# Optimization experiments

Hardware: AMD Instinct MI355X
Metric: run time of the kernel (lower is better)

The kernel has to match this reference:

```python
import jax, jax.numpy as jnp
import numpy as np

B, N = 2, 1024
D, H, DK, L = 128, 8, 16, 4
K_GCN, K_LOC, COARSE = 16, 8, 512
EPS = 1e-5
SCALE = 1.0 / float(np.sqrt(DK))


def _dist2(q, r):
    # squared euclidean distances [Nq, Nr]; same ordering as torch.cdist for topk
    return jnp.sum(q * q, -1)[:, None] - 2.0 * (q @ r.T) + jnp.sum(r * r, -1)[None, :]


def _knn_self(coords, k):
    # knn_graph(loop=False): k nearest neighbors excluding self, per batch
    def one(c):
        d2 = _dist2(c, c) + jnp.eye(c.shape[0], dtype=c.dtype) * 1e10
        return jax.lax.top_k(-d2, k)[1]  # [N, k] source-node indices
    return jax.vmap(one)(coords)


def _gcn(x, idx, w, b, k):
    # PyG GCNConv with self-loops on a knn graph: target in-degree is uniformly k+1,
    # so gcn_norm reduces to mean over {self} U knn neighbors.
    nb = jax.vmap(lambda xb, ib: xb[ib])(x, idx)  # [B,N,k,C]
    agg = (x + nb.sum(2)) / float(k + 1)
    return agg @ w + b


def _ln(x, g, b):
    m = x.mean(-1, keepdims=True)
    v = ((x - m) ** 2).mean(-1, keepdims=True)
    return (x - m) * jax.lax.rsqrt(v + EPS) * g + b


def _neigh_mean(part, pred, k):
    # local_knn + mean over the k gathered partial neighbors
    def one(pb, qb):
        idx = jax.lax.top_k(-_dist2(qb, pb), k)[1]  # [Nq,k]
        return pb[idx].mean(1)                      # [Nq,3]
    return jax.vmap(one)(part, pred)


def _refine(part, pred, sw1, sb1, sw2, sb2, dw, db, cw, cb):
    # LocalRefineStage: seed MLP -> ConvTranspose1d(k=2,s=2) on length-1 seq -> 1x1 conv -> offsets
    nm = _neigh_mean(part, pred, K_LOC)
    comb = jnp.concatenate([pred, nm], -1)                          # [B,N,6]
    seed = jax.nn.relu(comb @ sw1 + sb1) @ sw2 + sb2                # [B,N,128]
    h = jax.nn.relu(jnp.einsum('bnc,cot->bnot', seed, dw) + db[:, None])  # [B,N,128,2]
    y = jnp.einsum('bnot,po->bntp', h, cw) + cb                     # [B,N,2,3]
    child = pred[:, :, None, :] + y
    return child.reshape(pred.shape[0], -1, 3)


def _forward(partial_coords, gcn_w0, gcn_b0, gcn_w1, gcn_b1, enc_fw, enc_fb,
             t_wq, t_bq, t_wk, t_bk, t_wv, t_bv, t_alpha,
             t_f1w, t_f1b, t_f2w, t_f2b, t_ln1g, t_ln1b, t_ln2g, t_ln2b,
             dec_w1, dec_b1, dec_w2, dec_b2,
             st_sw1, st_sb1, st_sw2, st_sb2, st_dw, st_db, st_cw, st_cb):
    coords = partial_coords
    # --- GraphEncoder ---
    idx = _knn_self(coords, K_GCN)
    x = jax.nn.relu(_gcn(coords, idx, gcn_w0, gcn_b0, K_GCN))
    x = jax.nn.relu(_gcn(x, idx, gcn_w1, gcn_b1, K_GCN))
    x = x @ enc_fw + enc_fb  # tokens [B,N,128]; bridge_in is Identity (128==128)
    # --- GeomMultiTokenTransformer ---
    # block-diagonal extraction of (coords coords^T) == per-batch dot-product bias
    G = jnp.einsum('bnc,bmc->bnm', coords, coords)
    for i in range(L):
        q = (x @ t_wq[i] + t_bq[i]).reshape(B, N, H, DK)
        k = (x @ t_wk[i] + t_bk[i]).reshape(B, N, H, DK)
        v = (x @ t_wv[i] + t_bv[i]).reshape(B, N, H, DK)
        scores = jnp.einsum('bnhd,bmhd->bhnm', q, k) * SCALE + (t_alpha[i] * G)[:, None]
        a = jax.nn.softmax(scores, axis=-1)
        attn = jnp.einsum('bhnm,bmhd->bnhd', a, v).reshape(B, N, D)
        x = _ln(x + attn, t_ln1g[i], t_ln1b[i])
        ff = jax.nn.relu(x @ t_f1w[i] + t_f1b[i]) @ t_f2w[i] + t_f2b[i]
        x = _ln(x + ff, t_ln2g[i], t_ln2b[i])
    # --- Snowflake3StageDecoder ---
    gc = x.mean(1)
    pts = (jax.nn.relu(gc @ dec_w1 + dec_b1) @ dec_w2 + dec_b2).reshape(B, COARSE, 3)
    for s in range(3):
        pts = _refine(coords, pts, st_sw1[s], st_sb1[s], st_sw2[s], st_sb2[s],
                      st_dw[s], st_db[s], st_cw[s], st_cb[s])
    return pts  # [B, 4096, 3]


def setup_inputs() -> dict:
    key = jax.random.key(0)
    it = iter(jax.random.split(key, 64))
    def w(*shape):
        return jax.random.normal(next(it), shape, dtype=jnp.float32) * 0.05
    z = lambda *s: jnp.zeros(s, dtype=jnp.float32)
    o = lambda *s: jnp.ones(s, dtype=jnp.float32)
    return {
        'partial_coords': jax.random.normal(next(it), (B, N, 3), dtype=jnp.float32),
        'gcn_w0': w(3, 64), 'gcn_b0': z(64),
        'gcn_w1': w(64, 128), 'gcn_b1': z(128),
        'enc_fw': w(128, 128), 'enc_fb': z(128),
        't_wq': w(L, D, D), 't_bq': z(L, D),
        't_wk': w(L, D, D), 't_bk': z(L, D),
        't_wv': w(L, D, D), 't_bv': z(L, D),
        't_alpha': jnp.full((L,), 0.1, dtype=jnp.float32),
        't_f1w': w(L, D, 4 * D), 't_f1b': z(L, 4 * D),
        't_f2w': w(L, 4 * D, D), 't_f2b': z(L, D),
        't_ln1g': o(L, D), 't_ln1b': z(L, D),
        't_ln2g': o(L, D), 't_ln2b': z(L, D),
        'dec_w1': w(128, 128), 'dec_b1': z(128),
        'dec_w2': w(128, 3 * COARSE), 'dec_b2': z(3 * COARSE),
        'st_sw1': w(3, 6, 128), 'st_sb1': z(3, 128),
        'st_sw2': w(3, 128, 128), 'st_sb2': z(3, 128),
        'st_dw': w(3, 128, 128, 2), 'st_db': z(3, 128),
        'st_cw': w(3, 3, 128), 'st_cb': z(3, 3),
    }


def reference(partial_coords, gcn_w0, gcn_b0, gcn_w1, gcn_b1, enc_fw, enc_fb,
              t_wq, t_bq, t_wk, t_bk, t_wv, t_bv, t_alpha,
              t_f1w, t_f1b, t_f2w, t_f2b, t_ln1g, t_ln1b, t_ln2g, t_ln2b,
              dec_w1, dec_b1, dec_w2, dec_b2,
              st_sw1, st_sb1, st_sw2, st_sb2, st_dw, st_db, st_cw, st_cb):
    return _forward(partial_coords, gcn_w0, gcn_b0, gcn_w1, gcn_b1, enc_fw, enc_fb,
                    t_wq, t_bq, t_wk, t_bk, t_wv, t_bv, t_alpha,
                    t_f1w, t_f1b, t_f2w, t_f2b, t_ln1g, t_ln1b, t_ln2g, t_ln2b,
                    dec_w1, dec_b1, dec_w2, dec_b2,
                    st_sw1, st_sb1, st_sw2, st_sb2, st_dw, st_db, st_cw, st_cb)
```

## Files before the change

### kernel.cpp

```cpp
#include <hip/hip_runtime.h>


#define B_ 2
#define N_ 1024
#define D_ 128
#define H_ 8
#define DK_ 16
#define L_ 4
#define KG_ 16
#define KLOC_ 8
#define COARSE_ 512
#define AW_ 8
#define KSP_ 4
#define PREC_ 17
#define QPL_ 4

static __device__ __forceinline__ float wave_sum(float v) {
    #pragma unroll
    for (int off = 32; off > 0; off >>= 1) v += __shfl_xor(v, off);
    return v;
}
static __device__ __forceinline__ float half_sum(float v) {
    #pragma unroll
    for (int off = 16; off > 0; off >>= 1) v += __shfl_xor(v, off);
    return v;
}

template <int CIN, bool RELU, bool BIAS_HALF>
static __device__ __forceinline__ float4 gemm_body(
        const float* __restrict__ X, const float* __restrict__ W,
        const float* __restrict__ bias, int wstride, int col0) {
    __shared__ float Xs[8 * CIN];
    __shared__ float Ws[64][128];
    int tid = threadIdx.x;
    int row0 = blockIdx.x * 8;
    constexpr int NX4 = 2 * CIN;
    {
        const float4* xg = (const float4*)(X + (size_t)row0 * CIN);
        float4* xs4 = (float4*)Xs;
        #pragma unroll
        for (int i = 0; i < (NX4 + 255) / 256; ++i) {
            int t = tid + i * 256;
            if ((NX4 % 256 == 0) || t < NX4) xs4[t] = xg[t];
        }
    }
    int col4 = (tid & 31) << 2;
    int rowl = tid >> 5;
    float4 acc;
    if (BIAS_HALF) {
        acc.x = bias[(col0 + col4) >> 1];
        acc.y = bias[(col0 + col4 + 1) >> 1];
        acc.z = bias[(col0 + col4 + 2) >> 1];
        acc.w = bias[(col0 + col4 + 3) >> 1];
    } else {
        acc = *(const float4*)(bias + col0 + col4);
    }
    for (int c0 = 0; c0 < CIN; c0 += 64) {
        __syncthreads();
        #pragma unroll
        for (int i = 0; i < 8; ++i) {
            int flat = tid + i * 256;
            int wr = flat >> 5, wc = (flat & 31) << 2;
            *(float4*)&Ws[wr][wc] =
                *(const float4*)(W + (size_t)(c0 + wr) * wstride + col0 + wc);
        }
        __syncthreads();
        const float* xrow = Xs + rowl * CIN + c0;
        #pragma unroll
        for (int c = 0; c < 64; ++c) {
            float xv = xrow[c];
            float4 w = *(const float4*)&Ws[c][col4];
            acc.x += xv * w.x; acc.y += xv * w.y;
            acc.z += xv * w.z; acc.w += xv * w.w;
        }
    }
    if (RELU) {
        acc.x = fmaxf(acc.x, 0.f); acc.y = fmaxf(acc.y, 0.f);
        acc.z = fmaxf(acc.z, 0.f); acc.w = fmaxf(acc.w, 0.f);
    }
    return acc;
}

template <int CIN, bool RELU, bool BIAS_HALF>
__global__ __launch_bounds__(256) void gemm128_kernel(
        const float* __restrict__ X, const float* __restrict__ W,
        const float* __restrict__ bias, float* __restrict__ Y,
        int wstride, int ystride) {
    int col0 = blockIdx.y * 128;
    float4 acc = gemm_body<CIN, RELU, BIAS_HALF>(X, W, bias, wstride, col0);
    int col4 = (threadIdx.x & 31) << 2;
    int row = blockIdx.x * 8 + (threadIdx.x >> 5);
    *(float4*)(Y + (size_t)row * ystride + col0 + col4) = acc;
}

__global__ __launch_bounds__(256) void gemm_gcn_kernel(
        const float* __restrict__ x64, const int* __restrict__ knn,
        const float* __restrict__ W, const float* __restrict__ bias,
        float* __restrict__ Y) {
    __shared__ float Xs[8 * 64];
    __shared__ float Ws[64][128];
    int tid = threadIdx.x;
    int row0 = blockIdx.x * 8;
    #pragma unroll
    for (int i = 0; i < 2; ++i) {
        int idx = tid + i * 256;
        int r = idx >> 6, c = idx & 63;
        int row = row0 + r;
        int b = row >> 10;
        const int* id = knn + (size_t)row * KG_;
        float val = x64[(size_t)row * 64 + c];
        #pragma unroll
        for (int j = 0; j < KG_; ++j)
            val += x64[((size_t)(b << 10) + id[j]) * 64 + c];
        Xs[idx] = val * (1.0f / (KG_ + 1));
    }
    int col4 = (tid & 31) << 2;
    int rowl = tid >> 5;
    float4 acc = *(const float4*)(bias + col4);
    __syncthreads();
    #pragma unroll
    for (int i = 0; i < 8; ++i) {
        int flat = tid + i * 256;
        int wr = flat >> 5, wc = (flat & 31) << 2;
        *(float4*)&Ws[wr][wc] = *(const float4*)(W + (size_t)wr * 128 + wc);
    }
    __syncthreads();
    const float* xrow = Xs + rowl * 64;
    #pragma unroll
    for (int c = 0; c < 64; ++c) {
        float xv = xrow[c];
        float4 w = *(const float4*)&Ws[c][col4];
        acc.x += xv * w.x; acc.y += xv * w.y;
        acc.z += xv * w.z; acc.w += xv * w.w;
    }
    acc.x = fmaxf(acc.x, 0.f); acc.y = fmaxf(acc.y, 0.f);
    acc.z = fmaxf(acc.z, 0.f); acc.w = fmaxf(acc.w, 0.f);
    int row = row0 + rowl;
    *(float4*)(Y + (size_t)row * 128 + col4) = acc;
}

__global__ __launch_bounds__(256) void gcnlin0_kernel(
        const float* __restrict__ coords, const int* __restrict__ knn,
        const float* __restrict__ w0, const float* __restrict__ b0,
        float* __restrict__ x64) {
    int lane = threadIdx.x & 63;
    int row = blockIdx.x * 4 + (threadIdx.x >> 6);
    int b = row >> 10;
    const float* cb = coords + (size_t)(b << 10) * 3;
    int n = row & (N_ - 1);
    float ax = cb[n * 3], ay = cb[n * 3 + 1], az = cb[n * 3 + 2];
    const int* id = knn + (size_t)row * KG_;
    #pragma unroll
    for (int j = 0; j < KG_; ++j) {
        int m = id[j];
        ax += cb[m * 3]; ay += cb[m * 3 + 1]; az += cb[m * 3 + 2];
    }
    float s = 1.0f / (KG_ + 1);
    ax *= s; ay *= s; az *= s;
    float acc = b0[lane] + ax * w0[lane] + ay * w0[64 + lane] + az * w0[128 + lane];
    x64[(size_t)row * 64 + lane] = fmaxf(acc, 0.f);
}

template <int CIN>
__global__ __launch_bounds__(256) void gemm_ln_kernel(
        const float* __restrict__ X, const float* __restrict__ W,
        const float* __restrict__ bias, const float* __restrict__ res,
        const float* __restrict__ g, const float* __restrict__ bt,
        float* __restrict__ Y) {
    float4 acc = gemm_body<CIN, false, false>(X, W, bias, 128, 0);
    int col4 = (threadIdx.x & 31) << 2;
    int row = blockIdx.x * 8 + (threadIdx.x >> 5);
    float4 r = *(const float4*)(res + (size_t)row * D_ + col4);
    acc.x += r.x; acc.y += r.y; acc.z += r.z; acc.w += r.w;
    float mean = half_sum(acc.x + acc.y + acc.z + acc.w) * (1.0f / D_);
    float dx = acc.x - mean, dy = acc.y - mean, dz = acc.z - mean, dw = acc.w - mean;
    float var = half_sum(dx * dx + dy * dy + dz * dz + dw * dw) * (1.0f / D_);
    float rstd = rsqrtf(var + 1e-5f);
    float4 gv = *(const float4*)(g + col4);
    float4 bv = *(const float4*)(bt + col4);
    float4 o;
    o.x = dx * rstd * gv.x + bv.x;
    o.y = dy * rstd * gv.y + bv.y;
    o.z = dz * rstd * gv.z + bv.z;
    o.w = dw * rstd * gv.w + bv.w;
    *(float4*)(Y + (size_t)row * D_ + col4) = o;
}

__global__ __launch_bounds__(256) void gemm_ffn1_kernel(
        const float* __restrict__ pp, const float* __restrict__ xin,
        const float* __restrict__ g, const float* __restrict__ bt,
        const float* __restrict__ W, const float* __restrict__ bias,
        float* __restrict__ xln, float* __restrict__ Y) {
    __shared__ float Xs[8 * 128];
    __shared__ float Ws[64][128];
    int tid = threadIdx.x;
    int row0 = blockIdx.x * 8;
    int col0 = blockIdx.y * 128;
    int col4 = (tid & 31) << 2;
    int rowl = tid >> 5;
    {
        int row = row0 + rowl;
        int b = row >> 10, n = row & (N_ - 1);
        int h = col4 >> 4, d0 = col4 & 15;
        const float* p = pp + (((size_t)(b * 8 + h) * N_ + n) * KSP_) * PREC_;
        float gsum = 0.f, a0 = 0.f, a1 = 0.f, a2 = 0.f, a3 = 0.f;
        #pragma unroll
        for (int s = 0; s < KSP_; ++s) {
            const float* ps = p + s * PREC_;
            gsum += ps[0];
            a0 += ps[1 + d0]; a1 += ps[2 + d0]; a2 += ps[3 + d0]; a3 += ps[4 + d0];
        }
        float inv = 1.0f / gsum;
        float4 xv = *(const float4*)(xin + (size_t)row * D_ + col4);
        float v0 = a0 * inv + xv.x;
        float v1 = a1 * inv + xv.y;
        float v2 = a2 * inv + xv.z;
        float v3 = a3 * inv + xv.w;
        float mean = half_sum(v0 + v1 + v2 + v3) * (1.0f / D_);
        float dx = v0 - mean, dy = v1 - mean, dz = v2 - mean, dw = v3 - mean;
        float var = half_sum(dx * dx + dy * dy + dz * dz + dw * dw) * (1.0f / D_);
        float rstd = rsqrtf(var + 1e-5f);
        float4 gv = *(const float4*)(g + col4);
        float4 bv = *(const float4*)(bt + col4);
        float4 o;
        o.x = dx * rstd * gv.x + bv.x;
        o.y = dy * rstd * gv.y + bv.y;
        o.z = dz * rstd * gv.z + bv.z;
        o.w = dw * rstd * gv.w + bv.w;
        *(float4*)&Xs[rowl * 128 + col4] = o;
        if (blockIdx.y == 0)
            *(float4*)(xln + (size_t)row * D_ + col4) = o;
    }
    float4 acc = *(const float4*)(bias + col0 + col4);
    for (int c0 = 0; c0 < 128; c0 += 64) {
        __syncthreads();
        #pragma unroll
        for (int i = 0; i < 8; ++i) {
            int flat = tid + i * 256;
            int wr = flat >> 5, wc = (flat & 31) << 2;
            *(float4*)&Ws[wr][wc] =
                *(const float4*)(W + (size_t)(c0 + wr) * 512 + col0 + wc);
        }
        __syncthreads();
        const float* xrow = Xs + rowl * 128 + c0;
        #pragma unroll
        for (int c = 0; c < 64; ++c) {
            float xv = xrow[c];
            float4 w = *(const float4*)&Ws[c][col4];
            acc.x += xv * w.x; acc.y += xv * w.y;
            acc.z += xv * w.z; acc.w += xv * w.w;
        }
    }
    acc.x = fmaxf(acc.x, 0.f); acc.y = fmaxf(acc.y, 0.f);
    acc.z = fmaxf(acc.z, 0.f); acc.w = fmaxf(acc.w, 0.f);
    int row = row0 + rowl;
    *(float4*)(Y + (size_t)row * 512 + col0 + col4) = acc;
}

__global__ __launch_bounds__(256) void qkv3_kernel(
        const float* __restrict__ X,
        const float* __restrict__ Wq, const float* __restrict__ bq,
        const float* __restrict__ Wk, const float* __restrict__ bk,
        const float* __restrict__ Wv, const float* __restrict__ bv,
        float* __restrict__ Q, float* __restrict__ K, float* __restrict__ V) {
    const float* W; const float* bias; float* Y;
    if (blockIdx.y == 0)      { W = Wq; bias = bq; Y = Q; }
    else if (blockIdx.y == 1) { W = Wk; bias = bk; Y = K; }
    else                      { W = Wv; bias = bv; Y = V; }
    float4 acc = gemm_body<128, false, false>(X, W, bias, 128, 0);
    int col4 = (threadIdx.x & 31) << 2;
    int row = blockIdx.x * 8 + (threadIdx.x >> 5);
    int b = row >> 10, n = row & (N_ - 1);
    int h = col4 >> 4, d = col4 & 15;
    *(float4*)(Y + (((size_t)(b * 8 + h) * N_ + n) << 4) + d) = acc;
}

__global__ __launch_bounds__(256) void knn_fused_kernel(
        const float* __restrict__ coords, int* __restrict__ knn) {
    __shared__ float4 sc[N_];
    int wid = threadIdx.x >> 6;
    int lane = threadIdx.x & 63;
    size_t q = (size_t)blockIdx.x * 4 + wid;
    int b = (int)(q >> 10), n = (int)(q & (N_ - 1));
    const float* cb = coords + (size_t)b * N_ * 3;
    for (int i = threadIdx.x; i < N_; i += 256) {
        float x = cb[i * 3], y = cb[i * 3 + 1], z = cb[i * 3 + 2];
        sc[i] = make_float4(x, y, z, x * x + y * y + z * z);
    }
    __syncthreads();
    float4 qc = sc[n];
    float qx = qc.x, qy = qc.y, qz = qc.z, q2 = qc.w;
    float ld[16];
    #pragma unroll
    for (int j = 0; j < 16; ++j) {
        int m = (j << 6) | lane;
        float4 c = sc[m];
        float dot = qx * c.x + qy * c.y + qz * c.z;
        float d = (q2 - 2.0f * dot) + c.w;
        ld[j] = (m == n) ? 3e38f : d;
    }
    int* o = knn + q * KG_;
    #pragma unroll
    for (int r = 0; r < KG_; ++r) {
        float dm = ld[0]; int im = lane;
        #pragma unroll
        for (int j = 1; j < 16; ++j) {
            int mj = (j << 6) | lane;
            bool lt = (ld[j] < dm) || (ld[j] == dm && mj < im);
            dm = lt ? ld[j] : dm; im = lt ? mj : im;
        }
        #pragma unroll
        for (int off = 32; off > 0; off >>= 1) {
            float d2 = __shfl_xor(dm, off); int i2 = __shfl_xor(im, off);
            bool lt = (d2 < dm) || (d2 == dm && i2 < im);
            dm = lt ? d2 : dm; im = lt ? i2 : im;
        }
        if (lane == 0) o[r] = im;
        if ((im & 63) == lane) {
            #pragma unroll
            for (int j = 0; j < 16; ++j) if ((im >> 6) == j) ld[j] = 3e38f;
        }
    }
}

__global__ __launch_bounds__(256) void loc_fused_kernel(
        const float* __restrict__ part, const float* __restrict__ pred,
        const float* __restrict__ sw1, const float* __restrict__ sb1,
        float* __restrict__ seedh, int Nq) {
    __shared__ float4 sc[N_];
    int wid = threadIdx.x >> 6;
    int lane = threadIdx.x & 63;
    size_t q = (size_t)blockIdx.x * 4 + wid;
    int b = (int)(q / Nq);
    const float* pb = part + (size_t)b * N_ * 3;
    for (int i = threadIdx.x; i < N_; i += 256) {
        float x = pb[i * 3], y = pb[i * 3 + 1], z = pb[i * 3 + 2];
        sc[i] = make_float4(x, y, z, x * x + y * y + z * z);
    }
    __syncthreads();
    const float* pr = pred + q * 3;
    float qx = pr[0], qy = pr[1], qz = pr[2];
    float q2 = qx * qx + qy * qy + qz * qz;
    float ld[16];
    #pragma unroll
    for (int j = 0; j < 16; ++j) {
        int m = (j << 6) | lane;
        float4 c = sc[m];
        float dot = qx * c.x + qy * c.y + qz * c.z;
        ld[j] = (q2 - 2.0f * dot) + c.w;
    }
    float sx = 0.f, sy = 0.f, sz = 0.f;
    #pragma unroll
    for (int r = 0; r < KLOC_; ++r) {
        float dm = ld[0]; int im = lane;
        #pragma unroll
        for (int j = 1; j < 16; ++j) {
            int mj = (j << 6) | lane;
            bool lt = (ld[j] < dm) || (ld[j] == dm && mj < im);
            dm = lt ? ld[j] : dm; im = lt ? mj : im;
        }
        #pragma unroll
        for (int off = 32; off > 0; off >>= 1) {
            float d2 = __shfl_xor(dm, off); int i2 = __shfl_xor(im, off);
            bool lt = (d2 < dm) || (d2 == dm && i2 < im);
            dm = lt ? d2 : dm; im = lt ? i2 : im;
        }
        float4 w = sc[im];
        sx += w.x; sy += w.y; sz += w.z;
        if ((im & 63) == lane) {
            #pragma unroll
            for (int j = 0; j < 16; ++j) if ((im >> 6) == j) ld[j] = 3e38f;
        }
    }
    float comb[6];
    comb[0] = qx; comb[1] = qy; comb[2] = qz;
    comb[3] = sx * (1.0f / KLOC_);
    comb[4] = sy * (1.0f / KLOC_);
    comb[5] = sz * (1.0f / KLOC_);
    float* so = seedh + q * 128;
    #pragma unroll
    for (int half = 0; half < 2; ++half) {
        int c = lane + half * 64;
        float acc = sb1[c];
        #pragma unroll
        for (int i = 0; i < 6; ++i) acc += comb[i] * sw1[i * 128 + c];
        so[c] = fmaxf(acc, 0.f);
    }
}

__global__ __launch_bounds__(256) void refine_tail_kernel(
        const float* __restrict__ seedh,
        const float* __restrict__ sw2, const float* __restrict__ sb2,
        const float* __restrict__ dw, const float* __restrict__ db,
        const float* __restrict__ cw, const float* __restrict__ cb,
        const float* __restrict__ pred, float* __restrict__ outp) {
    __shared__ float Xs[8 * 128];
    __shared__ float Ws[64][128];
    __shared__ float Sd[8 * 128];
    __shared__ float Hb[8 * 256];
    int tid = threadIdx.x;
    int row0 = blockIdx.x * 8;
    int col4 = (tid & 31) << 2;
    int rowl = tid >> 5;
    {
        const float4* xg = (const float4*)(seedh + (size_t)row0 * 128);
        float4* xs4 = (float4*)Xs;
        xs4[tid] = xg[tid];
    }
    float4 acc = *(const float4*)(sb2 + col4);
    for (int c0 = 0; c0 < 128; c0 += 64) {
        __syncthreads();
        #pragma unroll
        for (int i = 0; i < 8; ++i) {
            int flat = tid + i * 256;
            int wr = flat >> 5, wc = (flat & 31) << 2;
            *(float4*)&Ws[wr][wc] =
                *(const float4*)(sw2 + (size_t)(c0 + wr) * 128 + wc);
        }
        __syncthreads();
        const float* xrow = Xs + rowl * 128 + c0;
        #pragma unroll
        for (int c = 0; c < 64; ++c) {
            float xv = xrow[c];
            float4 w = *(const float4*)&Ws[c][col4];
            acc.x += xv * w.x; acc.y += xv * w.y;
            acc.z += xv * w.z; acc.w += xv * w.w;
        }
    }
    __syncthreads();
    *(float4*)&Sd[rowl * 128 + col4] = acc;
    #pragma unroll
    for (int panel = 0; panel < 2; ++panel) {
        int col0 = panel * 128;
        float4 a2;
        a2.x = db[(col0 + col4) >> 1];
        a2.y = db[(col0 + col4 + 1) >> 1];
        a2.z = db[(col0 + col4 + 2) >> 1];
        a2.w = db[(col0 + col4 + 3) >> 1];
        for (int c0 = 0; c0 < 128; c0 += 64) {
            __syncthreads();
            #pragma unroll
            for (int i = 0; i < 8; ++i) {
                int flat = tid + i * 256;
                int wr = flat >> 5, wc = (flat & 31) << 2;
                *(float4*)&Ws[wr][wc] =
                    *(const float4*)(dw + (size_t)(c0 + wr) * 256 + col0 + wc);
            }
            __syncthreads();
            const float* xrow = Sd + rowl * 128 + c0;
            #pragma unroll
            for (int c = 0; c < 64; ++c) {
                float xv = xrow[c];
                float4 w = *(const float4*)&Ws[c][col4];
                a2.x += xv * w.x; a2.y += xv * w.y;
                a2.z += xv * w.z; a2.w += xv * w.w;
            }
        }
        a2.x = fmaxf(a2.x, 0.f); a2.y = fmaxf(a2.y, 0.f);
        a2.z = fmaxf(a2.z, 0.f); a2.w = fmaxf(a2.w, 0.f);
        __syncthreads();
        *(float4*)&Hb[rowl * 256 + col0 + col4] = a2;
    }
    __syncthreads();
    if (tid < 48) {
        int r = tid / 6, rem = tid % 6;
        int t = rem / 3, p = rem % 3;
        const float* hr = Hb + r * 256;
        float a = cb[p];
        #pragma unroll 4
        for (int o = 0; o < 128; ++o) a += hr[o * 2 + t] * cw[p * 128 + o];
        size_t row = row0 + r;
        outp[row * 6 + t * 3 + p] = pred[row * 3 + p] + a;
    }
}

__global__ __launch_bounds__(256) void dec12_kernel(
        const float* __restrict__ gc,
        const float* __restrict__ w1, const float* __restrict__ b1,
        const float* __restrict__ w2, const float* __restrict__ b2,
        float* __restrict__ pts0) {
    __shared__ float gcs[128];
    __shared__ float dech[128];
    int tid = threadIdx.x;
    int row = blockIdx.x / 6;
    int colb = (blockIdx.x % 6) * 256;
    if (tid < 128) gcs[tid] = gc[row * 128 + tid];
    __syncthreads();
    if (tid < 128) {
        float a = b1[tid];
        #pragma unroll 4
        for (int c = 0; c < 128; ++c) a += gcs[c] * w1[c * 128 + tid];
        dech[tid] = fmaxf(a, 0.f);
    }
    __syncthreads();
    int col = colb + tid;
    float a = b2[col];
    #pragma unroll 4
    for (int c = 0; c < 128; ++c) a += dech[c] * w2[(size_t)c * 1536 + col];
    pts0[(size_t)row * 1536 + col] = a;
}

__global__ __launch_bounds__(512) void attn_part(
        const float* __restrict__ q,
        const float* __restrict__ k,
        const float* __restrict__ v,
        const float* __restrict__ coords,
        const float* __restrict__ alphap, int layer,
        float* __restrict__ pp) {
    __shared__ float smem[10304];
    float* kst = smem;
    float* vst = smem + 4096;
    float* ssum = smem;
    float* sacc = smem + 2048;
    int bh = blockIdx.x & 15;
    int t = blockIdx.x >> 4;
    int ks = t & (KSP_ - 1);
    int nb = t >> 2;
    int b = bh >> 3;
    int wid = threadIdx.x >> 6;
    int lane = threadIdx.x & 63;
    float alpha = alphap[layer];
    {
        const float4* kg = (const float4*)(k + (((size_t)bh * N_ + ks * 256) << 4));
        const float4* vg = (const float4*)(v + (((size_t)bh * N_ + ks * 256) << 4));
        float4* ks4 = (float4*)kst;
        float4* vs4 = (float4*)vst;
        #pragma unroll
        for (int i = 0; i < 2; ++i) {
            int idx = threadIdx.x + i * 512;
            ks4[idx] = kg[idx];
            vs4[idx] = vg[idx];
        }
    }
    int n0 = nb * 256 + lane;
    const float* cb = coords + (size_t)b * N_ * 3;
    float qv[QPL_][DK_];
    float cx[QPL_], cy[QPL_], cz[QPL_];
    #pragma unroll
    for (int u = 0; u < QPL_; ++u) {
        const float* qp = q + (((size_t)bh * N_ + n0 + u * 64) << 4);
        #pragma unroll
        for (int d = 0; d < DK_; ++d) qv[u][d] = qp[d];
        int nn = n0 + u * 64;
        cx[u] = cb[nn * 3]; cy[u] = cb[nn * 3 + 1]; cz[u] = cb[nn * 3 + 2];
    }
    float sm[QPL_];
    float acc[QPL_][DK_];
    #pragma unroll
    for (int u = 0; u < QPL_; ++u) {
        sm[u] = 0.f;
        #pragma unroll
        for (int d = 0; d < DK_; ++d) acc[u][d] = 0.f;
    }
    __syncthreads();
    int mbase = ks * 256 + wid * 32;
    int lbase = wid * 32;
    #pragma unroll 2
    for (int j = 0; j < 32; ++j) {
        float kk[16];
        {
            const float4* kr = (const float4*)(kst + ((lbase + j) << 4));
            *(float4*)&kk[0] = kr[0]; *(float4*)&kk[4] = kr[1];
            *(float4*)&kk[8] = kr[2]; *(float4*)&kk[12] = kr[3];
        }
        int m = mbase + j;
        float wx = cb[m * 3], wy = cb[m * 3 + 1], wz = cb[m * 3 + 2];
        float p[QPL_];
        #pragma unroll
        for (int u = 0; u < QPL_; ++u) {
            float dot = 0.f;
            #pragma unroll
            for (int d = 0; d < DK_; ++d) dot += qv[u][d] * kk[d];
            p[u] = __expf(dot * 0.25f + alpha * (wx * cx[u] + wy * cy[u] + wz * cz[u]));
            sm[u] += p[u];
        }
        float vv[16];
        {
            const float4* vr = (const float4*)(vst + ((lbase + j) << 4));
            *(float4*)&vv[0] = vr[0]; *(float4*)&vv[4] = vr[1];
            *(float4*)&vv[8] = vr[2]; *(float4*)&vv[12] = vr[3];
        }
        #pragma unroll
        for (int u = 0; u < QPL_; ++u)
            #pragma unroll
            for (int d = 0; d < DK_; ++d) acc[u][d] += p[u] * vv[d];
    }
    __syncthreads();
    #pragma unroll
    for (int u = 0; u < QPL_; ++u) ssum[wid * 256 + u * 64 + lane] = sm[u];
    int qi = threadIdx.x & 63;
    int dq = threadIdx.x >> 6;
    #pragma unroll
    for (int r = 0; r < QPL_; ++r) {
        #pragma unroll
        for (int d = 0; d < DK_; ++d) sacc[lane * 129 + wid * DK_ + d] = acc[r][d];
        __syncthreads();
        int n = nb * 256 + r * 64 + qi;
        float* o = pp + (((size_t)bh * N_ + n) * KSP_ + ks) * PREC_;
        if (dq == 0) {
            float gsum = 0.f;
            #pragma unroll
            for (int w = 0; w < AW_; ++w) gsum += ssum[w * 256 + r * 64 + qi];
            o[0] = gsum;
        }
        #pragma unroll
        for (int dd = 0; dd < 2; ++dd) {
            int d = dq * 2 + dd;
            float a = 0.f;
            #pragma unroll
            for (int w = 0; w < AW_; ++w) a += sacc[qi * 129 + w * DK_ + d];
            o[1 + d] = a;
        }
        __syncthreads();
    }
}

__global__ void colmean_kernel(const float* __restrict__ x,
                               float* __restrict__ gc) {
    int b = blockIdx.x;
    int d = threadIdx.x & 127;
    int sl = threadIdx.x >> 7;
    __shared__ float part[4][128];
    float s = 0.f;
    const float* xb = x + (size_t)b * N_ * D_;
    for (int n = sl * 256; n < sl * 256 + 256; ++n) s += xb[(size_t)n * D_ + d];
    part[sl][d] = s;
    __syncthreads();
    if (sl == 0)
        gc[b * D_ + d] = (part[0][d] + part[1][d] + part[2][d] + part[3][d]) * (1.0f / N_);
}

static inline int cdiv(int a, int b) { return (a + b - 1) / b; }

extern "C" void kernel_launch(void* const* d_in, const int* in_sizes, int n_in,
                              void* d_out, int out_size, void* d_ws, size_t ws_size,
                              hipStream_t stream) {
    (void)in_sizes; (void)n_in; (void)out_size; (void)ws_size;
    const float* coords = (const float*)d_in[0];
    const float* gcn_w0 = (const float*)d_in[1];
    const float* gcn_b0 = (const float*)d_in[2];
    const float* gcn_w1 = (const float*)d_in[3];
    const float* gcn_b1 = (const float*)d_in[4];
    const float* enc_fw = (const float*)d_in[5];
    const float* enc_fb = (const float*)d_in[6];
    const float* t_wq   = (const float*)d_in[7];
    const float* t_bq   = (const float*)d_in[8];
    const float* t_wk   = (const float*)d_in[9];
    const float* t_bk   = (const float*)d_in[10];
    const float* t_wv   = (const float*)d_in[11];
    const float* t_bv   = (const float*)d_in[12];
    const float* t_alpha= (const float*)d_in[13];
    const float* t_f1w  = (const float*)d_in[14];
    const float* t_f1b  = (const float*)d_in[15];
    const float* t_f2w  = (const float*)d_in[16];
    const float* t_f2b  = (const float*)d_in[17];
    const float* t_ln1g = (const float*)d_in[18];
    const float* t_ln1b = (const float*)d_in[19];
    const float* t_ln2g = (const float*)d_in[20];
    const float* t_ln2b = (const float*)d_in[21];
    const float* dec_w1 = (const float*)d_in[22];
    const float* dec_b1 = (const float*)d_in[23];
    const float* dec_w2 = (const float*)d_in[24];
    const float* dec_b2 = (const float*)d_in[25];
    const float* st_sw1 = (const float*)d_in[26];
    const float* st_sb1 = (const float*)d_in[27];
    const float* st_sw2 = (const float*)d_in[28];
    const float* st_sb2 = (const float*)d_in[29];
    const float* st_dw  = (const float*)d_in[30];
    const float* st_db  = (const float*)d_in[31];
    const float* st_cw  = (const float*)d_in[32];
    const float* st_cb  = (const float*)d_in[33];
    float* out = (float*)d_out;

    char* ws = (char*)d_ws;
    size_t off = 0;
    auto alloc = [&](size_t bytes) -> void* {
        void* p = ws + off;
        off += (bytes + 255) & ~(size_t)255;
        return p;
    };
    int*   knn   = (int*)  alloc((size_t)B_ * N_ * KG_ * 4);
    float* app   = (float*)alloc((size_t)B_ * H_ * N_ * KSP_ * PREC_ * 4);
    float* x64   = (float*)alloc((size_t)B_ * N_ * 64 * 4);
    float* xb    = (float*)alloc((size_t)B_ * N_ * D_ * 4);
    float* x     = (float*)alloc((size_t)B_ * N_ * D_ * 4);
    float* q     = (float*)alloc((size_t)B_ * N_ * D_ * 4);
    float* k     = (float*)alloc((size_t)B_ * N_ * D_ * 4);
    float* v     = (float*)alloc((size_t)B_ * N_ * D_ * 4);
    float* ffh   = (float*)alloc((size_t)B_ * N_ * 512 * 4);
    float* gc    = (float*)alloc((size_t)B_ * D_ * 4);
    float* pts0  = (float*)alloc((size_t)B_ * COARSE_ * 3 * 4);
    float* pts1  = (float*)alloc((size_t)B_ * 1024 * 3 * 4);
    float* pts2  = (float*)alloc((size_t)B_ * 2048 * 3 * 4);
    float* seedh = (float*)alloc((size_t)B_ * 2048 * 128 * 4);

    const int rows = B_ * N_;

    knn_fused_kernel<<<rows / 4, 256, 0, stream>>>(coords, knn);
    gcnlin0_kernel<<<rows / 4, 256, 0, stream>>>(coords, knn, gcn_w0, gcn_b0, x64);
    gemm_gcn_kernel<<<rows / 8, 256, 0, stream>>>(x64, knn, gcn_w1, gcn_b1, xb);
    gemm128_kernel<128, false, false><<<dim3(rows / 8, 1), 256, 0, stream>>>(xb, enc_fw, enc_fb, x, 128, 128);

    for (int i = 0; i < L_; ++i) {
        qkv3_kernel<<<dim3(rows / 8, 3), 256, 0, stream>>>(
            x, t_wq + i * 16384, t_bq + i * 128, t_wk + i * 16384, t_bk + i * 128,
            t_wv + i * 16384, t_bv + i * 128, q, k, v);
        attn_part<<<B_ * H_ * (N_ / 256) * KSP_, 512, 0, stream>>>(q, k, v, coords, t_alpha, i, app);
        gemm_ffn1_kernel<<<dim3(rows / 8, 4), 256, 0, stream>>>(
            app, x, t_ln1g + i * 128, t_ln1b + i * 128,
            t_f1w + i * 128 * 512, t_f1b + i * 512, xb, ffh);
        gemm_ln_kernel<512><<<rows / 8, 256, 0, stream>>>(ffh, t_f2w + i * 512 * 128, t_f2b + i * 128, xb, t_ln2g + i * 128, t_ln2b + i * 128, x);
    }

    colmean_kernel<<<B_, 512, 0, stream>>>(x, gc);
    dec12_kernel<<<12, 256, 0, stream>>>(gc, dec_w1, dec_b1, dec_w2, dec_b2, pts0);

    const float* pred = pts0;
    float* outs[3] = { pts1, pts2, out };
    int Nq = COARSE_;
    for (int s = 0; s < 3; ++s) {
        int srows = B_ * Nq;
        loc_fused_kernel<<<srows / 4, 256, 0, stream>>>(
            coords, pred, st_sw1 + s * 6 * 128, st_sb1 + s * 128, seedh, Nq);
        refine_tail_kernel<<<srows / 8, 256, 0, stream>>>(
            seedh, st_sw2 + s * 128 * 128, st_sb2 + s * 128,
            st_dw + s * 128 * 256, st_db + s * 128,
            st_cw + s * 3 * 128, st_cb + s * 3, pred, outs[s]);
        pred = outs[s];
        Nq <<= 1;
    }
}
```

Measured before the change: 380.7 us.

## Fuse knn with GCN layer0, encoder chain with QKV, and FFN2+LN with next QKV

Folds neighbor-coordinate aggregation into the knn selection kernel, fuses GCN layer 1, encoder linear and the first QKV projection into one kernel, and moves each later layer's QKV projection into the FFN2+LayerNorm kernel. This removes several launches and round trips of intermediates through global memory. In exchange, the fused kernels run QKV on only 256 blocks instead of 768 and serialise more GEMMs per block. The inner loop unroll also drops from full to 4, which may lower ILP.

```diff
diff --git a/kernel.cpp b/kernel.cpp
--- a/kernel.cpp
+++ b/kernel.cpp
@@ -15,92 +15,119 @@
 #define PREC_ 17
 #define QPL_ 4
 
-static __device__ __forceinline__ float wave_sum(float v) {
-    #pragma unroll
-    for (int off = 32; off > 0; off >>= 1) v += __shfl_xor(v, off);
-    return v;
-}
 static __device__ __forceinline__ float half_sum(float v) {
     #pragma unroll
     for (int off = 16; off > 0; off >>= 1) v += __shfl_xor(v, off);
     return v;
 }
 
-template <int CIN, bool RELU, bool BIAS_HALF>
-static __device__ __forceinline__ float4 gemm_body(
-        const float* __restrict__ X, const float* __restrict__ W,
-        const float* __restrict__ bias, int wstride, int col0) {
-    __shared__ float Xs[8 * CIN];
-    __shared__ float Ws[64][128];
-    int tid = threadIdx.x;
-    int row0 = blockIdx.x * 8;
-    constexpr int NX4 = 2 * CIN;
-    {
-        const float4* xg = (const float4*)(X + (size_t)row0 * CIN);
-        float4* xs4 = (float4*)Xs;
-        #pragma unroll
-        for (int i = 0; i < (NX4 + 255) / 256; ++i) {
-            int t = tid + i * 256;
-            if ((NX4 % 256 == 0) || t < NX4) xs4[t] = xg[t];
-        }
-    }
-    int col4 = (tid & 31) << 2;
-    int rowl = tid >> 5;
-    float4 acc;
-    if (BIAS_HALF) {
-        acc.x = bias[(col0 + col4) >> 1];
-        acc.y = bias[(col0 + col4 + 1) >> 1];
-        acc.z = bias[(col0 + col4 + 2) >> 1];
-        acc.w = bias[(col0 + col4 + 3) >> 1];
-    } else {
-        acc = *(const float4*)(bias + col0 + col4);
-    }
+static __device__ __forceinline__ float4 lds_gemm(
+        const float* Xs, float* Ws, const float* __restrict__ W,
+        int wstride, int col0, float4 acc, int CIN,
+        int tid, int rowl, int col4) {
     for (int c0 = 0; c0 < CIN; c0 += 64) {
         __syncthreads();
         #pragma unroll
         for (int i = 0; i < 8; ++i) {
             int flat = tid + i * 256;
             int wr = flat >> 5, wc = (flat & 31) << 2;
-            *(float4*)&Ws[wr][wc] =
+            *(float4*)&Ws[wr * 128 + wc] =
                 *(const float4*)(W + (size_t)(c0 + wr) * wstride + col0 + wc);
         }
         __syncthreads();
         const float* xrow = Xs + rowl * CIN + c0;
-        #pragma unroll
+        #pragma unroll 4
         for (int c = 0; c < 64; ++c) {
             float xv = xrow[c];
-            float4 w = *(const float4*)&Ws[c][col4];
+            float4 w = *(const float4*)&Ws[c * 128 + col4];
             acc.x += xv * w.x; acc.y += xv * w.y;
             acc.z += xv * w.z; acc.w += xv * w.w;
         }
     }
-    if (RELU) {
-        acc.x = fmaxf(acc.x, 0.f); acc.y = fmaxf(acc.y, 0.f);
-        acc.z = fmaxf(acc.z, 0.f); acc.w = fmaxf(acc.w, 0.f);
-    }
     return acc;
 }
 
-template <int CIN, bool RELU, bool BIAS_HALF>
-__global__ __launch_bounds__(256) void gemm128_kernel(
-        const float* __restrict__ X, const float* __restrict__ W,
-        const float* __restrict__ bias, float* __restrict__ Y,
-        int wstride, int ystride) {
-    int col0 = blockIdx.y * 128;
-    float4 acc = gemm_body<CIN, RELU, BIAS_HALF>(X, W, bias, wstride, col0);
-    int col4 = (threadIdx.x & 31) << 2;
-    int row = blockIdx.x * 8 + (threadIdx.x >> 5);
-    *(float4*)(Y + (size_t)row * ystride + col0 + col4) = acc;
-}
-
-__global__ __launch_bounds__(256) void gemm_gcn_kernel(
+static __device__ __forceinline__ void qkv_write(
+        float* __restrict__ Y, int row, int col4, float4 acc) {
+    int b = row >> 10, n = row & (N_ - 1);
+    int h = col4 >> 4, d = col4 & 15;
+    *(float4*)(Y + (((size_t)(b * 8 + h) * N_ + n) << 4) + d) = acc;
+}
+
+__global__ __launch_bounds__(256) void knn_gcn0_kernel(
+        const float* __restrict__ coords,
+        const float* __restrict__ w0, const float* __restrict__ b0,
+        int* __restrict__ knn, float* __restrict__ x64) {
+    __shared__ float4 sc[N_];
+    int wid = threadIdx.x >> 6;
+    int lane = threadIdx.x & 63;
+    size_t q = (size_t)blockIdx.x * 4 + wid;
+    int b = (int)(q >> 10), n = (int)(q & (N_ - 1));
+    const float* cb = coords + (size_t)b * N_ * 3;
+    for (int i = threadIdx.x; i < N_; i += 256) {
+        float x = cb[i * 3], y = cb[i * 3 + 1], z = cb[i * 3 + 2];
+        sc[i] = make_float4(x, y, z, x * x + y * y + z * z);
+    }
+    __syncthreads();
+    float4 qc = sc[n];
+    float qx = qc.x, qy = qc.y, qz = qc.z, q2 = qc.w;
+    float ld[16];
+    #pragma unroll
+    for (int j = 0; j < 16; ++j) {
+        int m = (j << 6) | lane;
+        float4 c = sc[m];
+        float dot = qx * c.x + qy * c.y + qz * c.z;
+        float d = (q2 - 2.0f * dot) + c.w;
+        ld[j] = (m == n) ? 3e38f : d;
+    }
+    int* o = knn + q * KG_;
+    float ax = qx, ay = qy, az = qz;
+    #pragma unroll
+    for (int r = 0; r < KG_; ++r) {
+        float dm = ld[0]; int im = lane;
+        #pragma unroll
+        for (int j = 1; j < 16; ++j) {
+            int mj = (j << 6) | lane;
+            bool lt = (ld[j] < dm) || (ld[j] == dm && mj < im);
+            dm = lt ? ld[j] : dm; im = lt ? mj : im;
+        }
+        #pragma unroll
+        for (int off = 32; off > 0; off >>= 1) {
+            float d2 = __shfl_xor(dm, off); int i2 = __shfl_xor(im, off);
+            bool lt = (d2 < dm) || (d2 == dm && i2 < im);
+            dm = lt ? d2 : dm; im = lt ? i2 : im;
+        }
+        if (lane == 0) o[r] = im;
+        float4 w = sc[im];
+        ax += w.x; ay += w.y; az += w.z;
+        if ((im & 63) == lane) {
+            #pragma unroll
+            for (int j = 0; j < 16; ++j) if ((im >> 6) == j) ld[j] = 3e38f;
+        }
+    }
+    float s = 1.0f / (KG_ + 1);
+    ax *= s; ay *= s; az *= s;
+    float acc = b0[lane] + ax * w0[lane] + ay * w0[64 + lane] + az * w0[128 + lane];
+    x64[q * 64 + lane] = fmaxf(acc, 0.f);
+}
+
+__global__ __launch_bounds__(256) void enc_fused_kernel(
         const float* __restrict__ x64, const int* __restrict__ knn,
-        const float* __restrict__ W, const float* __restrict__ bias,
-        float* __restrict__ Y) {
-    __shared__ float Xs[8 * 64];
-    __shared__ float Ws[64][128];
+        const float* __restrict__ w1, const float* __restrict__ b1,
+        const float* __restrict__ enc_fw, const float* __restrict__ enc_fb,
+        const float* __restrict__ Wq, const float* __restrict__ bq,
+        const float* __restrict__ Wk, const float* __restrict__ bk,
+        const float* __restrict__ Wv, const float* __restrict__ bv,
+        float* __restrict__ x, float* __restrict__ Q,
+        float* __restrict__ K, float* __restrict__ V) {
+    __shared__ float Xs64[8 * 64];
+    __shared__ float Ws[64 * 128];
+    __shared__ float Xa[8 * 128];
+    __shared__ float Xe[8 * 128];
     int tid = threadIdx.x;
     int row0 = blockIdx.x * 8;
+    int col4 = (tid & 31) << 2;
+    int rowl = tid >> 5;
     #pragma unroll
     for (int i = 0; i < 2; ++i) {
         int idx = tid + i * 256;
@@ -112,64 +139,58 @@
         #pragma unroll
         for (int j = 0; j < KG_; ++j)
             val += x64[((size_t)(b << 10) + id[j]) * 64 + c];
-        Xs[idx] = val * (1.0f / (KG_ + 1));
-    }
+        Xs64[idx] = val * (1.0f / (KG_ + 1));
+    }
+    float4 a1 = *(const float4*)(b1 + col4);
+    a1 = lds_gemm(Xs64, Ws, w1, 128, 0, a1, 64, tid, rowl, col4);
+    a1.x = fmaxf(a1.x, 0.f); a1.y = fmaxf(a1.y, 0.f);
+    a1.z = fmaxf(a1.z, 0.f); a1.w = fmaxf(a1.w, 0.f);
+    __syncthreads();
+    *(float4*)&Xa[rowl * 128 + col4] = a1;
+    float4 a2 = *(const float4*)(enc_fb + col4);
+    a2 = lds_gemm(Xa, Ws, enc_fw, 128, 0, a2, 128, tid, rowl, col4);
+    int row = row0 + rowl;
+    *(float4*)(x + (size_t)row * D_ + col4) = a2;
+    __syncthreads();
+    *(float4*)&Xe[rowl * 128 + col4] = a2;
+    float4 aq = *(const float4*)(bq + col4);
+    aq = lds_gemm(Xe, Ws, Wq, 128, 0, aq, 128, tid, rowl, col4);
+    qkv_write(Q, row, col4, aq);
+    float4 ak = *(const float4*)(bk + col4);
+    ak = lds_gemm(Xe, Ws, Wk, 128, 0, ak, 128, tid, rowl, col4);
+    qkv_write(K, row, col4, ak);
+    float4 av = *(const float4*)(bv + col4);
+    av = lds_gemm(Xe, Ws, Wv, 128, 0, av, 128, tid, rowl, col4);
+    qkv_write(V, row, col4, av);
+}
+
+template <bool LAST>
+__global__ __launch_bounds__(256) void lnqkv_kernel(
+        const float* __restrict__ ffh,
+        const float* __restrict__ W2, const float* __restrict__ b2,
+        const float* __restrict__ res,
+        const float* __restrict__ g, const float* __restrict__ bt,
+        const float* __restrict__ Wq, const float* __restrict__ bq,
+        const float* __restrict__ Wk, const float* __restrict__ bk,
+        const float* __restrict__ Wv, const float* __restrict__ bv,
+        float* __restrict__ x, float* __restrict__ Q,
+        float* __restrict__ K, float* __restrict__ V) {
+    __shared__ float Xs[8 * 512];
+    __shared__ float Ws[64 * 128];
+    __shared__ float Xe[8 * 128];
+    int tid = threadIdx.x;
+    int row0 = blockIdx.x * 8;
     int col4 = (tid & 31) << 2;
     int rowl = tid >> 5;
-    float4 acc = *(const float4*)(bias + col4);
-    __syncthreads();
-    #pragma unroll
-    for (int i = 0; i < 8; ++i) {
-        int flat = tid + i * 256;
-        int wr = flat >> 5, wc = (flat & 31) << 2;
-        *(float4*)&Ws[wr][wc] = *(const float4*)(W + (size_t)wr * 128 + wc);
-    }
-    __syncthreads();
-    const float* xrow = Xs + rowl * 64;
-    #pragma unroll
-    for (int c = 0; c < 64; ++c) {
-        float xv = xrow[c];
-        float4 w = *(const float4*)&Ws[c][col4];
-        acc.x += xv * w.x; acc.y += xv * w.y;
-        acc.z += xv * w.z; acc.w += xv * w.w;
-    }
-    acc.x = fmaxf(acc.x, 0.f); acc.y = fmaxf(acc.y, 0.f);
-    acc.z = fmaxf(acc.z, 0.f); acc.w = fmaxf(acc.w, 0.f);
+    {
+        const float4* xg = (const float4*)(ffh + (size_t)row0 * 512);
+        float4* xs4 = (float4*)Xs;
+        #pragma unroll
+        for (int i = 0; i < 4; ++i) xs4[tid + i * 256] = xg[tid + i * 256];
+    }
+    float4 acc = *(const float4*)(b2 + col4);
+    acc = lds_gemm(Xs, Ws, W2, 128, 0, acc, 512, tid, rowl, col4);
     int row = row0 + rowl;
-    *(float4*)(Y + (size_t)row * 128 + col4) = acc;
-}
-
-__global__ __launch_bounds__(256) void gcnlin0_kernel(
-        const float* __restrict__ coords, const int* __restrict__ knn,
-        const float* __restrict__ w0, const float* __restrict__ b0,
-        float* __restrict__ x64) {
-    int lane = threadIdx.x & 63;
-    int row = blockIdx.x * 4 + (threadIdx.x >> 6);
-    int b = row >> 10;
-    const float* cb = coords + (size_t)(b << 10) * 3;
-    int n = row & (N_ - 1);
-    float ax = cb[n * 3], ay = cb[n * 3 + 1], az = cb[n * 3 + 2];
-    const int* id = knn + (size_t)row * KG_;
-    #pragma unroll
-    for (int j = 0; j < KG_; ++j) {
-        int m = id[j];
-        ax += cb[m * 3]; ay += cb[m * 3 + 1]; az += cb[m * 3 + 2];
-    }
-    float s = 1.0f / (KG_ + 1);
-    ax *= s; ay *= s; az *= s;
-    float acc = b0[lane] + ax * w0[lane] + ay * w0[64 + lane] + az * w0[128 + lane];
-    x64[(size_t)row * 64 + lane] = fmaxf(acc, 0.f);
-}
-
-template <int CIN>
-__global__ __launch_bounds__(256) void gemm_ln_kernel(
-        const float* __restrict__ X, const float* __restrict__ W,
-        const float* __restrict__ bias, const float* __restrict__ res,
-        const float* __restrict__ g, const float* __restrict__ bt,
-        float* __restrict__ Y) {
-    float4 acc = gemm_body<CIN, false, false>(X, W, bias, 128, 0);
-    int col4 = (threadIdx.x & 31) << 2;
-    int row = blockIdx.x * 8 + (threadIdx.x >> 5);
     float4 r = *(const float4*)(res + (size_t)row * D_ + col4);
     acc.x += r.x; acc.y += r.y; acc.z += r.z; acc.w += r.w;
     float mean = half_sum(acc.x + acc.y + acc.z + acc.w) * (1.0f / D_);
@@ -177,13 +198,26 @@
     float var = half_sum(dx * dx + dy * dy + dz * dz + dw * dw) * (1.0f / D_);
     float rstd = rsqrtf(var + 1e-5f);
     float4 gv = *(const float4*)(g + col4);
-    float4 bv = *(const float4*)(bt + col4);
+    float4 bv4 = *(const float4*)(bt + col4);
     float4 o;
-    o.x = dx * rstd * gv.x + bv.x;
-    o.y = dy * rstd * gv.y + bv.y;
-    o.z = dz * rstd * gv.z + bv.z;
-    o.w = dw * rstd * gv.w + bv.w;
-    *(float4*)(Y + (size_t)row * D_ + col4) = o;
+    o.x = dx * rstd * gv.x + bv4.x;
+    o.y = dy * rstd * gv.y + bv4.y;
+    o.z = dz * rstd * gv.z + bv4.z;
+    o.w = dw * rstd * gv.w + bv4.w;
+    *(float4*)(x + (size_t)row * D_ + col4) = o;
+    if (!LAST) {
+        __syncthreads();
+        *(float4*)&Xe[rowl * 128 + col4] = o;
+        float4 aq = *(const float4*)(bq + col4);
+        aq = lds_gemm(Xe, Ws, Wq, 128, 0, aq, 128, tid, rowl, col4);
+        qkv_write(Q, row, col4, aq);
+        float4 ak = *(const float4*)(bk + col4);
+        ak = lds_gemm(Xe, Ws, Wk, 128, 0, ak, 128, tid, rowl, col4);
+        qkv_write(K, row, col4, ak);
+        float4 av = *(const float4*)(bv + col4);
+        av = lds_gemm(Xe, Ws, Wv, 128, 0, av, 128, tid, rowl, col4);
+        qkv_write(V, row, col4, av);
+    }
 }
 
 __global__ __launch_bounds__(256) void gemm_ffn1_kernel(
@@ -192,7 +226,7 @@
         const float* __restrict__ W, const float* __restrict__ bias,
         float* __restrict__ xln, float* __restrict__ Y) {
     __shared__ float Xs[8 * 128];
-    __shared__ float Ws[64][128];
+    __shared__ float Ws[64 * 128];
     int tid = threadIdx.x;
     int row0 = blockIdx.x * 8;
     int col0 = blockIdx.y * 128;
@@ -232,95 +266,11 @@
             *(float4*)(xln + (size_t)row * D_ + col4) = o;
     }
     float4 acc = *(const float4*)(bias + col0 + col4);
-    for (int c0 = 0; c0 < 128; c0 += 64) {
-        __syncthreads();
-        #pragma unroll
-        for (int i = 0; i < 8; ++i) {
-            int flat = tid + i * 256;
-            int wr = flat >> 5, wc = (flat & 31) << 2;
-            *(float4*)&Ws[wr][wc] =
-                *(const float4*)(W + (size_t)(c0 + wr) * 512 + col0 + wc);
-        }
-        __syncthreads();
-        const float* xrow = Xs + rowl * 128 + c0;
-        #pragma unroll
-        for (int c = 0; c < 64; ++c) {
-            float xv = xrow[c];
-            float4 w = *(const float4*)&Ws[c][col4];
-            acc.x += xv * w.x; acc.y += xv * w.y;
-            acc.z += xv * w.z; acc.w += xv * w.w;
-        }
-    }
+    acc = lds_gemm(Xs, Ws, W, 512, col0, acc, 128, tid, rowl, col4);
     acc.x = fmaxf(acc.x, 0.f); acc.y = fmaxf(acc.y, 0.f);
     acc.z = fmaxf(acc.z, 0.f); acc.w = fmaxf(acc.w, 0.f);
     int row = row0 + rowl;
     *(float4*)(Y + (size_t)row * 512 + col0 + col4) = acc;
-}
-
-__global__ __launch_bounds__(256) void qkv3_kernel(
-        const float* __restrict__ X,
-        const float* __restrict__ Wq, const float* __restrict__ bq,
-        const float* __restrict__ Wk, const float* __restrict__ bk,
-        const float* __restrict__ Wv, const float* __restrict__ bv,
-        float* __restrict__ Q, float* __restrict__ K, float* __restrict__ V) {
-    const float* W; const float* bias; float* Y;
-    if (blockIdx.y == 0)      { W = Wq; bias = bq; Y = Q; }
-    else if (blockIdx.y == 1) { W = Wk; bias = bk; Y = K; }
-    else                      { W = Wv; bias = bv; Y = V; }
-    float4 acc = gemm_body<128, false, false>(X, W, bias, 128, 0);
-    int col4 = (threadIdx.x & 31) << 2;
-    int row = blockIdx.x * 8 + (threadIdx.x >> 5);
-    int b = row >> 10, n = row & (N_ - 1);
-    int h = col4 >> 4, d = col4 & 15;
-    *(float4*)(Y + (((size_t)(b * 8 + h) * N_ + n) << 4) + d) = acc;
-}
-
-__global__ __launch_bounds__(256) void knn_fused_kernel(
-        const float* __restrict__ coords, int* __restrict__ knn) {
-    __shared__ float4 sc[N_];
-    int wid = threadIdx.x >> 6;
-    int lane = threadIdx.x & 63;
-    size_t q = (size_t)blockIdx.x * 4 + wid;
-    int b = (int)(q >> 10), n = (int)(q & (N_ - 1));
-    const float* cb = coords + (size_t)b * N_ * 3;
-    for (int i = threadIdx.x; i < N_; i += 256) {
-        float x = cb[i * 3], y = cb[i * 3 + 1], z = cb[i * 3 + 2];
-        sc[i] = make_float4(x, y, z, x * x + y * y + z * z);
-    }
-    __syncthreads();
-    float4 qc = sc[n];
-    float qx = qc.x, qy = qc.y, qz = qc.z, q2 = qc.w;
-    float ld[16];
-    #pragma unroll
-    for (int j = 0; j < 16; ++j) {
-        int m = (j << 6) | lane;
-        float4 c = sc[m];
-        float dot = qx * c.x + qy * c.y + qz * c.z;
-        float d = (q2 - 2.0f * dot) + c.w;
-        ld[j] = (m == n) ? 3e38f : d;
-    }
-    int* o = knn + q * KG_;
-    #pragma unroll
-    for (int r = 0; r < KG_; ++r) {
-        float dm = ld[0]; int im = lane;
-        #pragma unroll
-        for (int j = 1; j < 16; ++j) {
-            int mj = (j << 6) | lane;
-            bool lt = (ld[j] < dm) || (ld[j] == dm && mj < im);
-            dm = lt ? ld[j] : dm; im = lt ? mj : im;
-        }
-        #pragma unroll
-        for (int off = 32; off > 0; off >>= 1) {
-            float d2 = __shfl_xor(dm, off); int i2 = __shfl_xor(im, off);
-            bool lt = (d2 < dm) || (d2 == dm && i2 < im);
-            dm = lt ? d2 : dm; im = lt ? i2 : im;
-        }
-        if (lane == 0) o[r] = im;
-        if ((im & 63) == lane) {
-            #pragma unroll
-            for (int j = 0; j < 16; ++j) if ((im >> 6) == j) ld[j] = 3e38f;
-        }
-    }
 }
 
 __global__ __launch_bounds__(256) void loc_fused_kernel(
@@ -395,7 +345,7 @@
         const float* __restrict__ cw, const float* __restrict__ cb,
         const float* __restrict__ pred, float* __restrict__ outp) {
     __shared__ float Xs[8 * 128];
-    __shared__ float Ws[64][128];
+    __shared__ float Ws[64 * 128];
     __shared__ float Sd[8 * 128];
     __shared__ float Hb[8 * 256];
     int tid = threadIdx.x;
@@ -408,25 +358,7 @@
         xs4[tid] = xg[tid];
     }
     float4 acc = *(const float4*)(sb2 + col4);
-    for (int c0 = 0; c0 < 128; c0 += 64) {
-        __syncthreads();
-        #pragma unroll
-        for (int i = 0; i < 8; ++i) {
-            int flat = tid + i * 256;
-            int wr = flat >> 5, wc = (flat & 31) << 2;
-            *(float4*)&Ws[wr][wc] =
-                *(const float4*)(sw2 + (size_t)(c0 + wr) * 128 + wc);
-        }
-        __syncthreads();
-        const float* xrow = Xs + rowl * 128 + c0;
-        #pragma unroll
-        for (int c = 0; c < 64; ++c) {
-            float xv = xrow[c];
-            float4 w = *(const float4*)&Ws[c][col4];
-            acc.x += xv * w.x; acc.y += xv * w.y;
-            acc.z += xv * w.z; acc.w += xv * w.w;
-        }
-    }
+    acc = lds_gemm(Xs, Ws, sw2, 128, 0, acc, 128, tid, rowl, col4);
     __syncthreads();
     *(float4*)&Sd[rowl * 128 + col4] = acc;
     #pragma unroll
@@ -437,25 +369,7 @@
         a2.y = db[(col0 + col4 + 1) >> 1];
         a2.z = db[(col0 + col4 + 2) >> 1];
         a2.w = db[(col0 + col4 + 3) >> 1];
-        for (int c0 = 0; c0 < 128; c0 += 64) {
-            __syncthreads();
-            #pragma unroll
-            for (int i = 0; i < 8; ++i) {
-                int flat = tid + i * 256;
-                int wr = flat >> 5, wc = (flat & 31) << 2;
-                *(float4*)&Ws[wr][wc] =
-                    *(const float4*)(dw + (size_t)(c0 + wr) * 256 + col0 + wc);
-            }
-            __syncthreads();
-            const float* xrow = Sd + rowl * 128 + c0;
-            #pragma unroll
-            for (int c = 0; c < 64; ++c) {
-                float xv = xrow[c];
-                float4 w = *(const float4*)&Ws[c][col4];
-                a2.x += xv * w.x; a2.y += xv * w.y;
-                a2.z += xv * w.z; a2.w += xv * w.w;
-            }
-        }
+        a2 = lds_gemm(Sd, Ws, dw, 256, col0, a2, 128, tid, rowl, col4);
         a2.x = fmaxf(a2.x, 0.f); a2.y = fmaxf(a2.y, 0.f);
         a2.z = fmaxf(a2.z, 0.f); a2.w = fmaxf(a2.w, 0.f);
         __syncthreads();
@@ -629,8 +543,6 @@
     if (sl == 0)
         gc[b * D_ + d] = (part[0][d] + part[1][d] + part[2][d] + part[3][d]) * (1.0f / N_);
 }
-
-static inline int cdiv(int a, int b) { return (a + b - 1) / b; }
 
 extern "C" void kernel_launch(void* const* d_in, const int* in_sizes, int n_in,
                               void* d_out, int out_size, void* d_ws, size_t ws_size,
@@ -696,20 +608,30 @@
 
     const int rows = B_ * N_;
 
-    knn_fused_kernel<<<rows / 4, 256, 0, stream>>>(coords, knn);
-    gcnlin0_kernel<<<rows / 4, 256, 0, stream>>>(coords, knn, gcn_w0, gcn_b0, x64);
-    gemm_gcn_kernel<<<rows / 8, 256, 0, stream>>>(x64, knn, gcn_w1, gcn_b1, xb);
-    gemm128_kernel<128, false, false><<<dim3(rows / 8, 1), 256, 0, stream>>>(xb, enc_fw, enc_fb, x, 128, 128);
+    knn_gcn0_kernel<<<rows / 4, 256, 0, stream>>>(coords, gcn_w0, gcn_b0, knn, x64);
+    enc_fused_kernel<<<rows / 8, 256, 0, stream>>>(
+        x64, knn, gcn_w1, gcn_b1, enc_fw, enc_fb,
+        t_wq, t_bq, t_wk, t_bk, t_wv, t_bv, x, q, k, v);
 
     for (int i = 0; i < L_; ++i) {
-        qkv3_kernel<<<dim3(rows / 8, 3), 256, 0, stream>>>(
-            x, t_wq + i * 16384, t_bq + i * 128, t_wk + i * 16384, t_bk + i * 128,
-            t_wv + i * 16384, t_bv + i * 128, q, k, v);
         attn_part<<<B_ * H_ * (N_ / 256) * KSP_, 512, 0, stream>>>(q, k, v, coords, t_alpha, i, app);
         gemm_ffn1_kernel<<<dim3(rows / 8, 4), 256, 0, stream>>>(
             app, x, t_ln1g + i * 128, t_ln1b + i * 128,
             t_f1w + i * 128 * 512, t_f1b + i * 512, xb, ffh);
-        gemm_ln_kernel<512><<<rows / 8, 256, 0, stream>>>(ffh, t_f2w + i * 512 * 128, t_f2b + i * 128, xb, t_ln2g + i * 128, t_ln2b + i * 128, x);
+        if (i < L_ - 1) {
+            int j = i + 1;
+            lnqkv_kernel<false><<<rows / 8, 256, 0, stream>>>(
+                ffh, t_f2w + i * 512 * 128, t_f2b + i * 128, xb,
+                t_ln2g + i * 128, t_ln2b + i * 128,
+                t_wq + j * 16384, t_bq + j * 128, t_wk + j * 16384, t_bk + j * 128,
+                t_wv + j * 16384, t_bv + j * 128, x, q, k, v);
+        } else {
+            lnqkv_kernel<true><<<rows / 8, 256, 0, stream>>>(
+                ffh, t_f2w + i * 512 * 128, t_f2b + i * 128, xb,
+                t_ln2g + i * 128, t_ln2b + i * 128,
+                nullptr, nullptr, nullptr, nullptr, nullptr, nullptr,
+                x, nullptr, nullptr, nullptr);
+        }
     }
 
     colmean_kernel<<<B_, 512, 0, stream>>>(x, gc);
```

After: 404.7 us. 1.06x slower.
